# Kernel tuning notes

Hardware: AMD Instinct MI355X
Metric: run time of the kernel (lower is better)

Reference implementation:

```python
import jax, jax.numpy as jnp
import numpy as np

N, D = 16384, 256

def setup_inputs() -> dict:
    key = jax.random.key(0)
    k1, k2, k3 = jax.random.split(key, 3)
    X = jax.random.normal(k1, (N, D), dtype=jnp.float32)
    W = jax.random.normal(k2, (D, D), dtype=jnp.float32) * (1.0 / np.sqrt(D))
    b = jax.random.normal(k3, (D,), dtype=jnp.float32) * (1.0 / np.sqrt(D))
    return {"X": X, "W": W, "b": b}

def reference(X, W, b):
    # Step 1: bilinear attention A = X W X^T   (N, N) -- materialized as in original
    A = (X @ W) @ X.T
    # Step 2: context aggregation Z = A X      (N, D)
    Z = A @ X
    # Step 3: output head g = Z b              (N,)
    g = Z @ b
    return g
```

## Files before the change

### kernel.cpp

```cpp
#include <hip/hip_runtime.h>

#define NROWS 16384
#define DDIM  256
#define GBLK  2048
#define PBLK  8


#define SUB1  0
#define MAIN1 2048
#define GO1   2080
#define MAIN2 4128
#define GO2   4160
#define REFC  6208

__device__ __forceinline__ unsigned aload(const unsigned* p) {
    return __hip_atomic_load(p, __ATOMIC_RELAXED, __HIP_MEMORY_SCOPE_AGENT);
}
__device__ __forceinline__ float afload(const float* p) {
    return __hip_atomic_load(p, __ATOMIC_RELAXED, __HIP_MEMORY_SCOPE_AGENT);
}
__device__ __forceinline__ void astore(float* p, float v) {
    __hip_atomic_store(p, v, __ATOMIC_RELAXED, __HIP_MEMORY_SCOPE_AGENT);
}
__device__ __forceinline__ unsigned armw(unsigned* p) {
    return __hip_atomic_fetch_add(p, 1u, __ATOMIC_RELAXED, __HIP_MEMORY_SCOPE_AGENT);
}

__global__ __launch_bounds__(256, 8)
void fused(const float* __restrict__ X, const float* __restrict__ W,
           const float* __restrict__ b, float* __restrict__ p1,
           float* __restrict__ w2, unsigned* __restrict__ bars,
           float* __restrict__ g) {
    const int tid  = threadIdx.x;
    const int lane = tid & 63;
    const int wave = tid >> 6;
    const int bid  = blockIdx.x;

    __shared__ __align__(16) float sp[4 * DDIM];
    __shared__ __align__(16) float sv[DDIM];

    const float4* X4 = (const float4*)X;

    unsigned initv = 0;
    if (tid == 0) initv = aload(&bars[REFC]);

    {
        const float4 bf = ((const float4*)b)[lane];
        float4 vacc = make_float4(0.f, 0.f, 0.f, 0.f);
        const int row0 = bid * 8 + wave * 2;
        #pragma unroll
        for (int i = 0; i < 2; ++i) {
            const float4 xv = X4[(row0 + i) * 64 + lane];
            float t = xv.x * bf.x + xv.y * bf.y + xv.z * bf.z + xv.w * bf.w;
            #pragma unroll
            for (int off = 32; off; off >>= 1) t += __shfl_xor(t, off, 64);
            vacc.x += t * xv.x; vacc.y += t * xv.y;
            vacc.z += t * xv.z; vacc.w += t * xv.w;
        }
        ((float4*)&sp[wave * DDIM])[lane] = vacc;
        __syncthreads();
        const float s = sp[tid] + sp[DDIM + tid] + sp[2*DDIM + tid] + sp[3*DDIM + tid];
        astore(&p1[bid * DDIM + tid], s);
        if (bid == GBLK - 1) astore(&w2[tid], 0.f);
    }

    asm volatile("s_waitcnt vmcnt(0)" ::: "memory");
    __syncthreads();
    if (tid == 0) {
        const int grp = bid >> 5, mem = bid & 31;
        unsigned old = armw(&bars[SUB1 + grp * 32]);
        if (old - initv == 31u) armw(&bars[MAIN1]);
        unsigned spins = 0;
        if (mem == 0) {
            while (aload(&bars[MAIN1]) - initv < 64u) {
                __builtin_amdgcn_s_sleep(4);
                if (++spins > 400000u) break;
            }
            __hip_atomic_store(&bars[GO1 + grp * 32], initv + 1u,
                               __ATOMIC_RELAXED, __HIP_MEMORY_SCOPE_AGENT);
        } else {
            while (aload(&bars[GO1 + grp * 32]) - initv == 0u) {
                __builtin_amdgcn_s_sleep(4);
                if (++spins > 400000u) break;
            }
        }
    }
    __syncthreads();

    if (bid < PBLK) {
        const int c   = tid & 31;
        const int seg = tid >> 5;
        const float* base = p1 + (seg * 256) * DDIM + bid * 32 + c;
        float acc = 0.f;
        for (int it = 0; it < 256; it += 8) {
            const float t0 = afload(base + (it + 0) * DDIM);
            const float t1 = afload(base + (it + 1) * DDIM);
            const float t2 = afload(base + (it + 2) * DDIM);
            const float t3 = afload(base + (it + 3) * DDIM);
            const float t4 = afload(base + (it + 4) * DDIM);
            const float t5 = afload(base + (it + 5) * DDIM);
            const float t6 = afload(base + (it + 6) * DDIM);
            const float t7 = afload(base + (it + 7) * DDIM);
            acc += ((t0 + t1) + (t2 + t3)) + ((t4 + t5) + (t6 + t7));
        }
        sp[seg * 32 + c] = acc;
        __syncthreads();
        if (tid < 32) {
            float v = 0.f;
            #pragma unroll
            for (int s2 = 0; s2 < 8; ++s2) v += sp[s2 * 32 + tid];
            sv[tid] = v;
        }
        __syncthreads();
        const float4* W4  = (const float4*)W;
        const float4* sv4 = (const float4*)sv;
        float w2p = 0.f;
        #pragma unroll
        for (int k = 0; k < 8; ++k) {
            const float4 wv = W4[tid * 64 + bid * 8 + k];
            const float4 vv = sv4[k];
            w2p += wv.x * vv.x + wv.y * vv.y + wv.z * vv.z + wv.w * vv.w;
        }
        atomicAdd(&w2[tid], w2p);
    }

    asm volatile("s_waitcnt vmcnt(0)" ::: "memory");
    __syncthreads();
    if (tid == 0) {
        if (bid < PBLK) armw(&bars[MAIN2]);
        const int grp = bid >> 5, mem = bid & 31;
        unsigned spins = 0;
        if (mem == 0) {
            while (aload(&bars[MAIN2]) - initv < (unsigned)PBLK) {
                __builtin_amdgcn_s_sleep(4);
                if (++spins > 400000u) break;
            }
            __hip_atomic_store(&bars[GO2 + grp * 32], initv + 1u,
                               __ATOMIC_RELAXED, __HIP_MEMORY_SCOPE_AGENT);
        } else {
            while (aload(&bars[GO2 + grp * 32]) - initv == 0u) {
                __builtin_amdgcn_s_sleep(4);
                if (++spins > 400000u) break;
            }
        }
    }
    __syncthreads();

    {
        sv[tid] = afload(&w2[tid]);
        __syncthreads();
        const float4 wf = ((const float4*)sv)[lane];
        const int row0 = bid * 8 + wave * 2;
        #pragma unroll
        for (int i = 0; i < 2; ++i) {
            const float4 xv = X4[(row0 + i) * 64 + lane];
            float t = xv.x * wf.x + xv.y * wf.y + xv.z * wf.z + xv.w * wf.w;
            #pragma unroll
            for (int off = 32; off; off >>= 1) t += __shfl_xor(t, off, 64);
            if (lane == 0) g[row0 + i] = t;
        }
    }
}

extern "C" void kernel_launch(void* const* d_in, const int* in_sizes, int n_in,
                              void* d_out, int out_size, void* d_ws, size_t ws_size,
                              hipStream_t stream) {
    const float* X = (const float*)d_in[0];
    const float* W = (const float*)d_in[1];
    const float* b = (const float*)d_in[2];
    float* g = (float*)d_out;

    float*    p1   = (float*)d_ws;
    float*    w2   = p1 + GBLK * DDIM;
    unsigned* bars = (unsigned*)d_ws + 532480;

    fused<<<GBLK, 256, 0, stream>>>(X, W, b, p1, w2, bars, g);
}
```

Before: 78.38 us.

## Spread partial reduction over 64 blocks, prefetch X rows before second barrier

The middle reduction phase moves from 8 blocks, each summing a 32-column slice across all 2048 partials with strided scalar loads, to 64 blocks that each sum 32 partial rows with coalesced float4 loads and then compute a full W·v product. Their results are combined through atomicAdd into w2. The X rows for the final dot product are now loaded before the second grid barrier so their latency overlaps the wait. Spin-wait sleep intervals are halved. The cost is more atomics on w2 and a larger barrier count.

```diff
diff --git a/kernel.cpp b/kernel.cpp
--- a/kernel.cpp
+++ b/kernel.cpp
@@ -3,7 +3,7 @@
 #define NROWS 16384
 #define DDIM  256
 #define GBLK  2048
-#define PBLK  8
+#define RBLK  64
 
 
 #define SUB1  0
@@ -18,6 +18,13 @@
 }
 __device__ __forceinline__ float afload(const float* p) {
     return __hip_atomic_load(p, __ATOMIC_RELAXED, __HIP_MEMORY_SCOPE_AGENT);
+}
+__device__ __forceinline__ float4 afload4(const float4* p) {
+    const float* f = (const float*)p;
+    float4 r;
+    r.x = afload(f + 0); r.y = afload(f + 1);
+    r.z = afload(f + 2); r.w = afload(f + 3);
+    return r;
 }
 __device__ __forceinline__ void astore(float* p, float v) {
     __hip_atomic_store(p, v, __ATOMIC_RELAXED, __HIP_MEMORY_SCOPE_AGENT);
@@ -73,74 +80,66 @@
         unsigned spins = 0;
         if (mem == 0) {
             while (aload(&bars[MAIN1]) - initv < 64u) {
-                __builtin_amdgcn_s_sleep(4);
-                if (++spins > 400000u) break;
+                __builtin_amdgcn_s_sleep(2);
+                if (++spins > 800000u) break;
             }
             __hip_atomic_store(&bars[GO1 + grp * 32], initv + 1u,
                                __ATOMIC_RELAXED, __HIP_MEMORY_SCOPE_AGENT);
         } else {
             while (aload(&bars[GO1 + grp * 32]) - initv == 0u) {
-                __builtin_amdgcn_s_sleep(4);
-                if (++spins > 400000u) break;
+                __builtin_amdgcn_s_sleep(2);
+                if (++spins > 800000u) break;
             }
         }
     }
     __syncthreads();
 
-    if (bid < PBLK) {
-        const int c   = tid & 31;
-        const int seg = tid >> 5;
-        const float* base = p1 + (seg * 256) * DDIM + bid * 32 + c;
-        float acc = 0.f;
-        for (int it = 0; it < 256; it += 8) {
-            const float t0 = afload(base + (it + 0) * DDIM);
-            const float t1 = afload(base + (it + 1) * DDIM);
-            const float t2 = afload(base + (it + 2) * DDIM);
-            const float t3 = afload(base + (it + 3) * DDIM);
-            const float t4 = afload(base + (it + 4) * DDIM);
-            const float t5 = afload(base + (it + 5) * DDIM);
-            const float t6 = afload(base + (it + 6) * DDIM);
-            const float t7 = afload(base + (it + 7) * DDIM);
-            acc += ((t0 + t1) + (t2 + t3)) + ((t4 + t5) + (t6 + t7));
+    if (bid < RBLK) {
+        const float4* P4 = (const float4*)p1;
+        float4 acc = make_float4(0.f, 0.f, 0.f, 0.f);
+        const int rbase = bid * 32 + wave * 8;
+        #pragma unroll
+        for (int i = 0; i < 8; ++i) {
+            const float4 p = afload4(&P4[(rbase + i) * 64 + lane]);
+            acc.x += p.x; acc.y += p.y; acc.z += p.z; acc.w += p.w;
         }
-        sp[seg * 32 + c] = acc;
+        ((float4*)&sp[wave * DDIM])[lane] = acc;
         __syncthreads();
-        if (tid < 32) {
-            float v = 0.f;
-            #pragma unroll
-            for (int s2 = 0; s2 < 8; ++s2) v += sp[s2 * 32 + tid];
-            sv[tid] = v;
-        }
+        sv[tid] = sp[tid] + sp[DDIM + tid] + sp[2*DDIM + tid] + sp[3*DDIM + tid];
         __syncthreads();
         const float4* W4  = (const float4*)W;
         const float4* sv4 = (const float4*)sv;
-        float w2p = 0.f;
-        #pragma unroll
-        for (int k = 0; k < 8; ++k) {
-            const float4 wv = W4[tid * 64 + bid * 8 + k];
+        float y = 0.f;
+        #pragma unroll 8
+        for (int k = 0; k < 64; ++k) {
+            const float4 wv = W4[tid * 64 + k];
             const float4 vv = sv4[k];
-            w2p += wv.x * vv.x + wv.y * vv.y + wv.z * vv.z + wv.w * vv.w;
+            y += wv.x * vv.x + wv.y * vv.y + wv.z * vv.z + wv.w * vv.w;
         }
-        atomicAdd(&w2[tid], w2p);
+        atomicAdd(&w2[tid], y);
     }
+
+    const int row0 = bid * 8 + wave * 2;
+    const float4 xc0 = X4[(row0 + 0) * 64 + lane];
+    const float4 xc1 = X4[(row0 + 1) * 64 + lane];
 
     asm volatile("s_waitcnt vmcnt(0)" ::: "memory");
     __syncthreads();
     if (tid == 0) {
-        if (bid < PBLK) armw(&bars[MAIN2]);
+        if (bid < RBLK) armw(&bars[MAIN2]);
         const int grp = bid >> 5, mem = bid & 31;
         unsigned spins = 0;
         if (mem == 0) {
-            while (aload(&bars[MAIN2]) - initv < (unsigned)PBLK) {
-                __builtin_amdgcn_s_sleep(4);
-                if (++spins > 400000u) break;
+            while (aload(&bars[MAIN2]) - initv < (unsigned)RBLK) {
+                __builtin_amdgcn_s_sleep(2);
+                if (++spins > 800000u) break;
             }
             __hip_atomic_store(&bars[GO2 + grp * 32], initv + 1u,
                                __ATOMIC_RELAXED, __HIP_MEMORY_SCOPE_AGENT);
         } else {
             while (aload(&bars[GO2 + grp * 32]) - initv == 0u) {
-                __builtin_amdgcn_s_sleep(4);
-                if (++spins > 400000u) break;
+                __builtin_amdgcn_s_sleep(2);
+                if (++spins > 800000u) break;
             }
         }
     }
@@ -150,15 +149,14 @@
         sv[tid] = afload(&w2[tid]);
         __syncthreads();
         const float4 wf = ((const float4*)sv)[lane];
-        const int row0 = bid * 8 + wave * 2;
+        float t0 = xc0.x * wf.x + xc0.y * wf.y + xc0.z * wf.z + xc0.w * wf.w;
+        float t1 = xc1.x * wf.x + xc1.y * wf.y + xc1.z * wf.z + xc1.w * wf.w;
         #pragma unroll
-        for (int i = 0; i < 2; ++i) {
-            const float4 xv = X4[(row0 + i) * 64 + lane];
-            float t = xv.x * wf.x + xv.y * wf.y + xv.z * wf.z + xv.w * wf.w;
-            #pragma unroll
-            for (int off = 32; off; off >>= 1) t += __shfl_xor(t, off, 64);
-            if (lane == 0) g[row0 + i] = t;
+        for (int off = 32; off; off >>= 1) {
+            t0 += __shfl_xor(t0, off, 64);
+            t1 += __shfl_xor(t1, off, 64);
         }
+        if (lane == 0) { g[row0] = t0; g[row0 + 1] = t1; }
     }
 }
 
```

Result: slower. 83.18 us (+6.1%).
